# Optimization experiments

Measured on AMD Instinct MI355X. Metric: run time of the kernel, lower is better.

Reference implementation:

```python
import jax, jax.numpy as jnp
import numpy as np

B, T, H, D, L = 64, 256, 1024, 1024, 6  # batch, seq_len, hidden, input, num stacked cells


def setup_inputs() -> dict:
    key = jax.random.key(0)
    ks = jax.random.split(key, 8)
    std = 1.0 / H ** 0.5
    u = lambda k, s: jax.random.uniform(k, s, jnp.float32, -std, std)
    return {
        "x": jax.random.normal(ks[0], (B, T, D), jnp.float32),
        "h0": jax.random.normal(ks[1], (L, B, H), jnp.float32),
        "weight_ih": u(ks[2], (H, D)),   # present in module but unused on the h-provided path
        "bias_ih": u(ks[3], (H,)),
        "weight_hh": u(ks[4], (H, H)),
        "bias_bh": u(ks[5], (H,)),
        "w_out": u(ks[6], (1, H)),       # nn.Linear(hidden_size, 1)
        "b_out": u(ks[7], (1,)),
    }


def reference(x, h0, weight_ih, bias_ih, weight_hh, bias_bh, w_out, b_out):
    # Faithful to RNN_Flat.forward with h provided:
    #   for t: for l in 0..5: h[l] = tanh(h[l-1] @ Whh.T + b_ih + h[l] @ Whh.T + b_bh)
    # where for l=0, h[-1] is h[5] carried from the previous time step,
    # and x_t is never consumed on this code path.
    seq_len = x.shape[1]
    Whh_t = weight_hh.T

    def cell(prev, h_l):  # cell_hh: weight_hh used for both projections
        return jnp.tanh(prev @ Whh_t + bias_ih + h_l @ Whh_t + bias_bh)

    def step(h, _):
        prev = h[-1]  # in-place update semantics: layer 0 sees previous step's h[5]
        new = []
        for l in range(L):
            prev = cell(prev, h[l])
            new.append(prev)
        h_new = jnp.stack(new, axis=0)  # [L, B, H]
        return h_new, h_new[-1]

    h_final, top = jax.lax.scan(step, h0, None, length=seq_len)  # top: [T, B, H]
    seq = jnp.swapaxes(top, 0, 1)                                # [B, T, H]
    out = seq @ w_out.T + b_out                                  # [B, T, 1]
    return out, h_final
```

## Files before the change

### kernel.cpp

```cpp
#include <hip/hip_runtime.h>


#define BB 64
#define TT 256
#define HH 1024
#define LL 6
#define NG 8
#define GB 8
#define NQ 32
#define SJ 32
#define NTH 256

#define HSTATE_FLOATS (2ull * BB * LL * HH)
#define FLAGS_OFF   (HSTATE_FLOATS * 4)
#define NSLOTS      (1 + TT * LL)
#define FLAG_STRIDE 16
#define FLAGS_BYTES ((size_t)NSLOTS * NG * FLAG_STRIDE * 4)
#define PARTIAL_OFF (FLAGS_OFF + FLAGS_BYTES)

__global__ void __launch_bounds__(NTH, 1)
rnn_kernel(const float* __restrict__ h0,
           const float* __restrict__ Whh,
           const float* __restrict__ bias_ih,
           const float* __restrict__ bias_bh,
           const float* __restrict__ w_out,
           const float* __restrict__ b_out,
           float* hstate, unsigned* flags, float* partial,
           float* __restrict__ d_out)
{
    __shared__ float4 Wl4[256 * SJ];
    __shared__ float4 s4[GB * 64];

    const int tid = threadIdx.x;
    const int g   = blockIdx.x & 7;
    const int q   = blockIdx.x >> 3;
    const int gb  = g * GB;
    const int jl  = tid & 31;
    const int bl  = tid >> 5;
    const int jg  = q * SJ + jl;
    const int b   = gb + bl;

    for (int it = 0; it < 32; ++it) {
        int idx  = it * NTH + tid;
        int jrow = idx >> 8;
        int k4   = idx & 255;
        const float4* src = (const float4*)(Whh + (size_t)(q * SJ + jrow) * HH);
        Wl4[k4 * SJ + jrow] = src[k4];
    }

    const float bias_j = bias_ih[jg] + bias_bh[jg];
    const float wout_j = w_out[jg];
    const float bout   = b_out[0];

    for (int l = 0; l < LL; ++l)
        hstate[(((size_t)1 * BB + b) * LL + l) * HH + jg] =
            h0[((size_t)l * BB + b) * HH + jg];

    auto gbar = [&](int slot) {
        __syncthreads();
        if (tid == 0) {
            unsigned* f = flags + ((size_t)slot * NG + g) * FLAG_STRIDE;
            __hip_atomic_fetch_add(f, 1u, __ATOMIC_RELEASE, __HIP_MEMORY_SCOPE_AGENT);
            for (int w = 0; w < 50000; ++w) {
                if (__hip_atomic_load(f, __ATOMIC_ACQUIRE, __HIP_MEMORY_SCOPE_AGENT) >= NQ)
                    break;
                __builtin_amdgcn_s_sleep(2);
            }
        }
        __syncthreads();
    };

    gbar(0);

    for (int t = 0; t < TT; ++t) {
        const int pw = t & 1, pr = pw ^ 1;
        for (int l = 0; l < LL; ++l) {
            const int lp = (l == 0) ? (LL - 1) : (l - 1);
            const int pp = (l == 0) ? pr : pw;

            float acc = 0.f;
            for (int ch = 0; ch < 4; ++ch) {
#pragma unroll
                for (int r = 0; r < 2; ++r) {
                    int idx = tid + r * NTH;
                    int bb = idx >> 6, kk = idx & 63;
                    const float4* P  = (const float4*)(hstate +
                        (((size_t)pp * BB + gb + bb) * LL + lp) * HH + ch * 256);
                    const float4* Ho = (const float4*)(hstate +
                        (((size_t)pr * BB + gb + bb) * LL + l) * HH + ch * 256);
                    float4 a = P[kk], c = Ho[kk];
                    s4[idx] = make_float4(a.x + c.x, a.y + c.y, a.z + c.z, a.w + c.w);
                }
                __syncthreads();

                const float4* wbase = Wl4 + (size_t)ch * 64 * SJ;
#pragma unroll 8
                for (int kk = 0; kk < 64; ++kk) {
                    float4 w = wbase[kk * SJ + jl];
                    float4 x = s4[bl * 64 + kk];
                    acc = fmaf(w.x, x.x, fmaf(w.y, x.y,
                          fmaf(w.z, x.z, fmaf(w.w, x.w, acc))));
                }
                __syncthreads();
            }

            float y = tanhf(acc + bias_j);
            hstate[(((size_t)pw * BB + b) * LL + l) * HH + jg] = y;

            if (l == LL - 1) {
                float c = y * wout_j;
#pragma unroll
                for (int off = 16; off; off >>= 1) c += __shfl_down(c, off, 32);
                if ((tid & 31) == 0)
                    partial[(size_t)pw * BB * NQ + (size_t)b * NQ + q] = c;
            }
            if (t == TT - 1)
                d_out[(size_t)BB * TT + ((size_t)l * BB + b) * HH + jg] = y;

            gbar(1 + t * LL + l);

            if (l == LL - 1 && q == 0 && tid < GB) {
                int bo = gb + tid;
                float s = bout;
#pragma unroll
                for (int qq = 0; qq < NQ; ++qq)
                    s += partial[(size_t)pw * BB * NQ + (size_t)bo * NQ + qq];
                d_out[(size_t)bo * TT + t] = s;
            }
        }
    }
}

extern "C" void kernel_launch(void* const* d_in, const int* in_sizes, int n_in,
                              void* d_out, int out_size, void* d_ws, size_t ws_size,
                              hipStream_t stream) {
    const float* h0      = (const float*)d_in[1];
    const float* bias_ih = (const float*)d_in[3];
    const float* Whh     = (const float*)d_in[4];
    const float* bias_bh = (const float*)d_in[5];
    const float* w_out   = (const float*)d_in[6];
    const float* b_out   = (const float*)d_in[7];

    float*    hstate  = (float*)d_ws;
    unsigned* flags   = (unsigned*)((char*)d_ws + FLAGS_OFF);
    float*    partial = (float*)((char*)d_ws + PARTIAL_OFF);

    hipMemsetAsync(flags, 0, FLAGS_BYTES, stream);
    rnn_kernel<<<NG * NQ, NTH, 0, stream>>>(h0, Whh, bias_ih, bias_bh,
                                            w_out, b_out, hstate, flags, partial,
                                            (float*)d_out);
}
```

Measured before the change: 22.17 ms.

## Keep weight slices in registers, split K across warps, use per-block flag barrier

Each thread now holds a 32x float4 slice of its weight row in registers instead of staging the weight tile in LDS. The work is split along K across the eight 32-lane groups, and each thread accumulates all 8 batch rows. Partial sums are reduced with a cross-half shuffle and a small LDS buffer. The whole 8x1024 input is loaded in one pass, which removes the per-chunk syncthreads. The group barrier switches from a monotonically growing counter array to per-block epoch flags polled by a wave ballot, and the sleep is dropped. This costs many VGPRs (128 for the weights) and raises the risk of spilling.

```diff
diff --git a/kernel.cpp b/kernel.cpp
--- a/kernel.cpp
+++ b/kernel.cpp
@@ -13,10 +13,8 @@
 
 #define HSTATE_FLOATS (2ull * BB * LL * HH)
 #define FLAGS_OFF   (HSTATE_FLOATS * 4)
-#define NSLOTS      (1 + TT * LL)
-#define FLAG_STRIDE 16
-#define FLAGS_BYTES ((size_t)NSLOTS * NG * FLAG_STRIDE * 4)
-#define PARTIAL_OFF (FLAGS_OFF + FLAGS_BYTES)
+#define FLAGS_BYTES ((size_t)NG * NQ * 4)
+#define PARTIAL_OFF (FLAGS_OFF + 1024)
 
 __global__ void __launch_bounds__(NTH, 1)
 rnn_kernel(const float* __restrict__ h0,
@@ -28,49 +26,62 @@
            float* hstate, unsigned* flags, float* partial,
            float* __restrict__ d_out)
 {
-    __shared__ float4 Wl4[256 * SJ];
-    __shared__ float4 s4[GB * 64];
+    __shared__ float4 s4[GB * 256];
+    __shared__ float  pred[4][SJ][GB];
 
     const int tid = threadIdx.x;
     const int g   = blockIdx.x & 7;
     const int q   = blockIdx.x >> 3;
     const int gb  = g * GB;
     const int jl  = tid & 31;
-    const int bl  = tid >> 5;
+    const int ks  = tid >> 5;
+    const int wv  = tid >> 6;
     const int jg  = q * SJ + jl;
-    const int b   = gb + bl;
 
-    for (int it = 0; it < 32; ++it) {
-        int idx  = it * NTH + tid;
-        int jrow = idx >> 8;
-        int k4   = idx & 255;
-        const float4* src = (const float4*)(Whh + (size_t)(q * SJ + jrow) * HH);
-        Wl4[k4 * SJ + jrow] = src[k4];
+    float4 wreg[32];
+    {
+        const float4* wrow = (const float4*)(Whh + (size_t)jg * HH) + ks * 32;
+#pragma unroll
+        for (int r = 0; r < 32; ++r) wreg[r] = wrow[r];
     }
 
     const float bias_j = bias_ih[jg] + bias_bh[jg];
     const float wout_j = w_out[jg];
     const float bout   = b_out[0];
 
-    for (int l = 0; l < LL; ++l)
-        hstate[(((size_t)1 * BB + b) * LL + l) * HH + jg] =
-            h0[((size_t)l * BB + b) * HH + jg];
+    {
+        int bb = tid >> 5, k = q * SJ + (tid & 31);
+#pragma unroll
+        for (int l = 0; l < LL; ++l)
+            hstate[(((size_t)1 * BB + gb + bb) * LL + l) * HH + k] =
+                h0[((size_t)l * BB + gb + bb) * HH + k];
+    }
 
-    auto gbar = [&](int slot) {
+    unsigned* gflags = flags + g * NQ;
+    unsigned barno = 0;
+
+    auto gbar = [&]() {
+        ++barno;
         __syncthreads();
-        if (tid == 0) {
-            unsigned* f = flags + ((size_t)slot * NG + g) * FLAG_STRIDE;
-            __hip_atomic_fetch_add(f, 1u, __ATOMIC_RELEASE, __HIP_MEMORY_SCOPE_AGENT);
-            for (int w = 0; w < 50000; ++w) {
-                if (__hip_atomic_load(f, __ATOMIC_ACQUIRE, __HIP_MEMORY_SCOPE_AGENT) >= NQ)
-                    break;
-                __builtin_amdgcn_s_sleep(2);
+        if (tid == 0)
+            __hip_atomic_store(gflags + q, barno, __ATOMIC_RELEASE,
+                               __HIP_MEMORY_SCOPE_AGENT);
+        if (tid < 64) {
+            for (int w = 0; w < 30000; ++w) {
+                unsigned v = (tid < NQ)
+                    ? __hip_atomic_load(gflags + tid, __ATOMIC_RELAXED,
+                                        __HIP_MEMORY_SCOPE_AGENT)
+                    : barno;
+                if (!~__ballot(v >= barno)) break;
             }
+            if (tid == 0)
+                (void)__hip_atomic_load(gflags + q, __ATOMIC_ACQUIRE,
+                                        __HIP_MEMORY_SCOPE_AGENT);
         }
         __syncthreads();
     };
 
-    gbar(0);
+    gbar();
 
     for (int t = 0; t < TT; ++t) {
         const int pw = t & 1, pr = pw ^ 1;
@@ -78,46 +89,61 @@
             const int lp = (l == 0) ? (LL - 1) : (l - 1);
             const int pp = (l == 0) ? pr : pw;
 
-            float acc = 0.f;
-            for (int ch = 0; ch < 4; ++ch) {
+            const float* baseP = hstate + (((size_t)pp * BB + gb) * LL + lp) * HH;
+            const float* baseH = hstate + (((size_t)pr * BB + gb) * LL + l ) * HH;
+            float4 pa[8], ha[8];
 #pragma unroll
-                for (int r = 0; r < 2; ++r) {
-                    int idx = tid + r * NTH;
-                    int bb = idx >> 6, kk = idx & 63;
-                    const float4* P  = (const float4*)(hstate +
-                        (((size_t)pp * BB + gb + bb) * LL + lp) * HH + ch * 256);
-                    const float4* Ho = (const float4*)(hstate +
-                        (((size_t)pr * BB + gb + bb) * LL + l) * HH + ch * 256);
-                    float4 a = P[kk], c = Ho[kk];
-                    s4[idx] = make_float4(a.x + c.x, a.y + c.y, a.z + c.z, a.w + c.w);
+            for (int r = 0; r < 8; ++r) {
+                pa[r] = *(const float4*)(baseP + (size_t)r * LL * HH + tid * 4);
+                ha[r] = *(const float4*)(baseH + (size_t)r * LL * HH + tid * 4);
+            }
+#pragma unroll
+            for (int r = 0; r < 8; ++r)
+                s4[r * 256 + tid] = make_float4(pa[r].x + ha[r].x, pa[r].y + ha[r].y,
+                                                pa[r].z + ha[r].z, pa[r].w + ha[r].w);
+            __syncthreads();
+
+            float acc[GB];
+#pragma unroll
+            for (int b = 0; b < GB; ++b) acc[b] = 0.f;
+            const float4* xbase = s4 + ks * 32;
+#pragma unroll
+            for (int b = 0; b < GB; ++b) {
+#pragma unroll
+                for (int k4 = 0; k4 < 32; ++k4) {
+                    float4 x = xbase[b * 256 + k4];
+                    float4 w = wreg[k4];
+                    acc[b] = fmaf(w.x, x.x, fmaf(w.y, x.y,
+                             fmaf(w.z, x.z, fmaf(w.w, x.w, acc[b]))));
                 }
-                __syncthreads();
-
-                const float4* wbase = Wl4 + (size_t)ch * 64 * SJ;
-#pragma unroll 8
-                for (int kk = 0; kk < 64; ++kk) {
-                    float4 w = wbase[kk * SJ + jl];
-                    float4 x = s4[bl * 64 + kk];
-                    acc = fmaf(w.x, x.x, fmaf(w.y, x.y,
-                          fmaf(w.z, x.z, fmaf(w.w, x.w, acc))));
-                }
-                __syncthreads();
             }
 
-            float y = tanhf(acc + bias_j);
-            hstate[(((size_t)pw * BB + b) * LL + l) * HH + jg] = y;
+#pragma unroll
+            for (int b = 0; b < GB; ++b) acc[b] += __shfl_xor(acc[b], 32);
+            if ((tid & 63) < 32) {
+                float4* pr4 = (float4*)&pred[wv][jl][0];
+                pr4[0] = make_float4(acc[0], acc[1], acc[2], acc[3]);
+                pr4[1] = make_float4(acc[4], acc[5], acc[6], acc[7]);
+            }
+            __syncthreads();
+
+            const int bb = tid >> 5;
+            float ysum = pred[0][jl][bb] + pred[1][jl][bb]
+                       + pred[2][jl][bb] + pred[3][jl][bb];
+            float y = tanhf(ysum + bias_j);
+            hstate[(((size_t)pw * BB + gb + bb) * LL + l) * HH + jg] = y;
 
             if (l == LL - 1) {
                 float c = y * wout_j;
 #pragma unroll
                 for (int off = 16; off; off >>= 1) c += __shfl_down(c, off, 32);
-                if ((tid & 31) == 0)
-                    partial[(size_t)pw * BB * NQ + (size_t)b * NQ + q] = c;
+                if (jl == 0)
+                    partial[(size_t)pw * BB * NQ + (size_t)(gb + bb) * NQ + q] = c;
             }
             if (t == TT - 1)
-                d_out[(size_t)BB * TT + ((size_t)l * BB + b) * HH + jg] = y;
+                d_out[(size_t)BB * TT + ((size_t)l * BB + gb + bb) * HH + jg] = y;
 
-            gbar(1 + t * LL + l);
+            gbar();
 
             if (l == LL - 1 && q == 0 && tid < GB) {
                 int bo = gb + tid;
```

Result: slower. 25.42 ms (+14.7%).
